# Kernel tuning notes

Measured on AMD Instinct MI355X. Metric: run time of the kernel, lower is better.

Reference implementation:

```python
import jax, jax.numpy as jnp
import numpy as np

jax.config.update("jax_enable_x64", True)  # module does int64 wraparound hashing

# Derived from BloomFilter(num_items=10_000_000, false_positive_rate=0.01):
#   pre-round num_bits = ceil(1e7 * ln(100) / ln(2)^2) ~= 95,850,584
#   num_hashes = ceil(pre_round_bits / 1e7 * ln(2)) = 7
#   num_bits rounded up to power of two -> 2**27
NUM_BITS = 2 ** 27
BIT_MASK = NUM_BITS - 1
NUM_HASHES = 7
PRIME = 2654435761


def _hash(values):
    """(N,) int64 -> (N, k) bit positions. Matches torch: (v*PRIME + seed) & bit_mask
    (note Python precedence: & binds looser than +). int64 overflow wraps identically."""
    seeds = jnp.arange(NUM_HASHES, dtype=jnp.int64)
    return (values[:, None] * PRIME + seeds[None, :]) & BIT_MASK


def setup_inputs() -> dict:
    key = jax.random.key(0)
    k1, k2 = jax.random.split(key)
    add_values = jax.random.randint(k1, (4_000_000,), 0, 2**31 - 1, dtype=jnp.int64)
    query_values = jax.random.randint(k2, (8_000_000,), 0, 2**31 - 1, dtype=jnp.int64)
    return {"add_values": add_values, "query_values": query_values}


def reference(add_values, query_values):
    # Bit array of NUM_BITS bools. Semantically identical to the packed int64
    # bitset: word w, offset b in torch <-> flat index (w << 6) | b here, and a
    # bitwise-OR of single-bit masks is exactly an idempotent set-True scatter.
    bits = jnp.zeros((NUM_BITS,), dtype=bool)

    # add(): scatter-set all k hash positions of every inserted value
    add_pos = _hash(add_values)  # (M, k)
    bits = bits.at[add_pos.reshape(-1)].set(True)

    # contains(): gather k bits per query and AND-reduce
    q_pos = _hash(query_values)  # (N, k)
    return jnp.all(bits[q_pos], axis=1)  # (N,) bool
```

## Files before the change

kernel.cpp:

```cpp
#include <hip/hip_runtime.h>
#include <stdint.h>


#define NUM_BITS_LOG2 27
#define NUM_BITS (1u << NUM_BITS_LOG2)
#define BIT_MASK (NUM_BITS - 1u)
#define NUM_WORDS (NUM_BITS >> 6)
#define WORD_MASK (NUM_WORDS - 1u)
#define PRIME 2654435761u
#define H_WORDS (NUM_WORDS >> 2)

#define NBUCKETS 512
#define BKT_SHIFT (NUM_BITS_LOG2 - 9)
#define REGION_WORDS (1u << (BKT_SHIFT - 6))
#define H_WORDS_PER_REGION (REGION_WORDS / 4)
#define CAP 8688u
#define CHUNK 8192u

typedef int vint4 __attribute__((ext_vector_type(4)));
typedef unsigned long long vull2 __attribute__((ext_vector_type(2)));

#define WS_H_ONLY 20971520ull
#define WS_FULL   38766592ull

__global__ __launch_bounds__(512) void scatter_kernel(
    const int* __restrict__ vals, int n,
    uint32_t* __restrict__ lists, uint32_t* __restrict__ gcnt)
{
    __shared__ uint32_t hist[NBUCKETS];
    __shared__ uint32_t cur[NBUCKETS];
    __shared__ uint32_t gdelta[NBUCKETS];
    __shared__ uint32_t wsum[8];
    __shared__ uint32_t wexc[8];
    __shared__ uint32_t total_s;
    __shared__ uint32_t sortbuf[CHUNK];
    const uint32_t tid = threadIdx.x;
    const uint32_t lane = tid & 63u;
    const uint32_t wv = tid >> 6;
    const uint32_t un = (uint32_t)n;
    const uint32_t nchunks = (un + CHUNK - 1u) / CHUNK;

    for (uint32_t c = blockIdx.x; c < nchunks; c += gridDim.x) {
        const uint32_t base = c * CHUNK;
        const bool full = (base + CHUNK <= un);

        hist[tid] = 0u;
        __syncthreads();

        vint4 vv[4];
        if (full) {
            const vint4* src = (const vint4*)(vals + base);
            #pragma unroll
            for (int k = 0; k < 4; ++k) vv[k] = src[(uint32_t)k * 512u + tid];
            #pragma unroll
            for (int k = 0; k < 4; ++k) {
                #pragma unroll
                for (int j = 0; j < 4; ++j) {
                    uint32_t p = ((uint32_t)vv[k][j] * PRIME) & BIT_MASK;
                    uint32_t b1 = p >> BKT_SHIFT;
                    atomicAdd(&hist[b1], 1u);
                    uint32_t b2 = ((p + 6u) & BIT_MASK) >> BKT_SHIFT;
                    if (b2 != b1) {
                        uint32_t s2 = atomicAdd(&gcnt[b2], 1u);
                        if (s2 < CAP) lists[b2 * CAP + s2] = p;
                    }
                }
            }
        } else {
            #pragma unroll
            for (int k = 0; k < 16; ++k) {
                uint32_t idx = base + (uint32_t)k * 512u + tid;
                if (idx < un) {
                    uint32_t p = ((uint32_t)vals[idx] * PRIME) & BIT_MASK;
                    uint32_t b1 = p >> BKT_SHIFT;
                    atomicAdd(&hist[b1], 1u);
                    uint32_t b2 = ((p + 6u) & BIT_MASK) >> BKT_SHIFT;
                    if (b2 != b1) {
                        uint32_t s2 = atomicAdd(&gcnt[b2], 1u);
                        if (s2 < CAP) lists[b2 * CAP + s2] = p;
                    }
                }
            }
        }
        __syncthreads();

        const uint32_t c0 = hist[tid];
        uint32_t x = c0;
        #pragma unroll
        for (uint32_t d = 1; d < 64; d <<= 1) {
            uint32_t y = __shfl_up(x, d, 64);
            if (lane >= d) x += y;
        }
        if (lane == 63u) wsum[wv] = x;
        __syncthreads();
        if (wv == 0) {
            uint32_t t8 = (lane < 8u) ? wsum[lane] : 0u;
            #pragma unroll
            for (uint32_t d = 1; d < 8; d <<= 1) {
                uint32_t y = __shfl_up(t8, d, 64);
                if (lane >= d) t8 += y;
            }
            if (lane < 8u) wexc[lane] = t8 - wsum[lane];
        }
        __syncthreads();
        const uint32_t inc = x + wexc[wv];
        const uint32_t lb = inc - c0;
        if (tid == NBUCKETS - 1) total_s = inc;

        uint32_t go = c0 ? atomicAdd(&gcnt[tid], c0) : 0u;
        cur[tid] = lb;
        gdelta[tid] = tid * CAP + go - lb;
        __syncthreads();

        if (full) {
            #pragma unroll
            for (int k = 0; k < 4; ++k) {
                #pragma unroll
                for (int j = 0; j < 4; ++j) {
                    uint32_t p = ((uint32_t)vv[k][j] * PRIME) & BIT_MASK;
                    uint32_t b1 = p >> BKT_SHIFT;
                    uint32_t s = atomicAdd(&cur[b1], 1u);
                    sortbuf[s] = p;
                }
            }
        } else {
            #pragma unroll
            for (int k = 0; k < 16; ++k) {
                uint32_t idx = base + (uint32_t)k * 512u + tid;
                if (idx < un) {
                    uint32_t p = ((uint32_t)vals[idx] * PRIME) & BIT_MASK;
                    uint32_t b1 = p >> BKT_SHIFT;
                    uint32_t s = atomicAdd(&cur[b1], 1u);
                    sortbuf[s] = p;
                }
            }
        }
        __syncthreads();

        const uint32_t total = total_s;
        for (uint32_t i = tid; i < total; i += 512u) {
            uint32_t p = sortbuf[i];
            uint32_t b = p >> BKT_SHIFT;
            uint32_t dst = gdelta[b] + i;
            if (dst - b * CAP < CAP) lists[dst] = p;
        }
        __syncthreads();
    }
}

__device__ __forceinline__ void set_window(unsigned long long* bm, uint32_t p, uint32_t b) {
    int d = (int)((p - (b << BKT_SHIFT)) & BIT_MASK);
    if (d >= (1 << 26)) d -= (1 << 27);
    if (d < -6 || d >= (1 << BKT_SHIFT)) return;
    if (d < 0) {
        atomicOr(&bm[0], 0x7Full >> (uint32_t)(-d));
    } else {
        uint32_t w = (uint32_t)d >> 6, s = (uint32_t)d & 63u;
        atomicOr(&bm[w], 0x7Full << s);
        if (s > 57u) atomicOr(&bm[w + 1], 0x7Full >> (64u - s));
    }
}

__device__ __forceinline__ unsigned long long nib16(unsigned long long a) {
    unsigned long long t = a & (a >> 1);
    unsigned long long u = t & (t >> 2);
    u &= 0x1111111111111111ull;
    u |= u >> 3;  u &= 0x0303030303030303ull;
    u |= u >> 6;  u &= 0x000F000F000F000Full;
    u |= u >> 12; u &= 0x000000FF000000FFull;
    u |= u >> 24; return u & 0xFFFFull;
}

__global__ __launch_bounds__(512) void build_bitmap_kernel(
    const uint32_t* __restrict__ lists, const uint32_t* __restrict__ gcnt,
    unsigned long long* __restrict__ bits, unsigned long long* __restrict__ H)
{
    __shared__ unsigned long long bm[REGION_WORDS + 1];
    const uint32_t b = blockIdx.x, tid = threadIdx.x;
    for (uint32_t i = tid; i < REGION_WORDS + 1; i += 512) bm[i] = 0ull;
    __syncthreads();

    const uint32_t m = min(gcnt[b], CAP);
    const uint32_t base = b * CAP;
    for (uint32_t i = tid; i < m; i += 512) set_window(bm, lists[base + i], b);
    __syncthreads();

    const uint32_t out_base = b * REGION_WORDS;
    for (uint32_t i = tid; i < REGION_WORDS / 2; i += 512) {
        vull2 w; w[0] = bm[i * 2]; w[1] = bm[i * 2 + 1];
        *((vull2*)(bits + out_base) + i) = w;
    }
    const uint32_t h_base = b * H_WORDS_PER_REGION;
    for (uint32_t i = tid; i < H_WORDS_PER_REGION; i += 512) {
        unsigned long long hw = nib16(bm[i * 4])
                              | (nib16(bm[i * 4 + 1]) << 16)
                              | (nib16(bm[i * 4 + 2]) << 32)
                              | (nib16(bm[i * 4 + 3]) << 48);
        H[h_base + i] = hw;
    }
}

__device__ __forceinline__ int query_one_branchy(uint32_t v,
                                                 const unsigned long long* __restrict__ bits) {
    uint32_t p = (v * PRIME) & BIT_MASK;
    uint32_t w = p >> 6, s = p & 63u;
    unsigned long long lo = bits[w];
    unsigned long long win;
    if (s <= 57u) win = lo >> s;
    else win = (lo >> s) | (bits[(w + 1u) & WORD_MASK] << (64u - s));
    return ((win & 0x7Full) == 0x7Full) ? 1 : 0;
}

__global__ __launch_bounds__(256) void query_kernelH(
    const int* __restrict__ vals, int n,
    const unsigned long long* __restrict__ bits,
    const uint32_t* __restrict__ H32, int* __restrict__ out)
{
    int t = blockIdx.x * 256 + threadIdx.x;
    int base = t * 8;
    if (base + 7 < n) {
        vint4 v0 = __builtin_nontemporal_load((const vint4*)(vals + base));
        vint4 v1 = __builtin_nontemporal_load((const vint4*)(vals + base + 4));
        uint32_t p[8], pass[8];
        #pragma unroll
        for (int j = 0; j < 4; ++j) {
            p[j]     = ((uint32_t)v0[j] * PRIME) & BIT_MASK;
            p[j + 4] = ((uint32_t)v1[j] * PRIME) & BIT_MASK;
        }
        #pragma unroll
        for (int j = 0; j < 8; ++j) {
            uint32_t m = ((p[j] + 3u) & BIT_MASK) >> 2;
            pass[j] = (H32[m >> 5] >> (m & 31u)) & 1u;
        }
        unsigned long long lo[8], hi[8];
        uint32_t w[8], s[8];
        #pragma unroll
        for (int j = 0; j < 8; ++j) {
            w[j] = p[j] >> 6; s[j] = p[j] & 63u;
            lo[j] = 0ull; hi[j] = 0ull;
            if (pass[j]) lo[j] = bits[w[j]];
        }
        #pragma unroll
        for (int j = 0; j < 8; ++j) {
            if (pass[j] && s[j] > 57u)
                hi[j] = bits[(w[j] + 1u) & WORD_MASK];
        }
        vint4 r0, r1;
        #pragma unroll
        for (int j = 0; j < 8; ++j) {
            unsigned long long win = (lo[j] >> s[j]) | ((hi[j] << 1) << (63u - s[j]));
            int r = ((win & 0x7Full) == 0x7Full) ? 1 : 0;
            if (j < 4) r0[j] = r; else r1[j - 4] = r;
        }
        __builtin_nontemporal_store(r0, (vint4*)(out + base));
        __builtin_nontemporal_store(r1, (vint4*)(out + base + 4));
    } else {
        for (int j = base; j < n; ++j)
            out[j] = query_one_branchy((uint32_t)vals[j], bits);
    }
}

__global__ __launch_bounds__(256) void zero_bits_kernel(vull2* __restrict__ bits, int n2) {
    int i = blockIdx.x * 256 + threadIdx.x;
    if (i < n2) { vull2 z = {0ull, 0ull}; __builtin_nontemporal_store(z, &bits[i]); }
}

__device__ __forceinline__ void insert_one_atomic(uint32_t v,
                                                  unsigned long long* __restrict__ bits) {
    uint32_t p = (v * PRIME) & BIT_MASK;
    uint32_t w = p >> 6, s = p & 63u;
    atomicOr(bits + w, 0x7Full << s);
    if (s > 57u) atomicOr(bits + ((w + 1u) & WORD_MASK), 0x7Full >> (64u - s));
}

__global__ __launch_bounds__(256) void insert_atomic_kernel(const int* __restrict__ vals, int n,
                                                            unsigned long long* __restrict__ bits) {
    int t = blockIdx.x * 256 + threadIdx.x;
    int base = t * 4;
    if (base + 3 < n) {
        vint4 v = __builtin_nontemporal_load((const vint4*)vals + t);
        insert_one_atomic((uint32_t)v.x, bits);
        insert_one_atomic((uint32_t)v.y, bits);
        insert_one_atomic((uint32_t)v.z, bits);
        insert_one_atomic((uint32_t)v.w, bits);
    } else {
        for (int j = base; j < n; ++j) insert_one_atomic((uint32_t)vals[j], bits);
    }
}

__global__ __launch_bounds__(256) void build_h_kernel(
    const unsigned long long* __restrict__ bits, unsigned long long* __restrict__ H)
{
    uint32_t i = blockIdx.x * 256 + threadIdx.x;
    const vull2* b2 = (const vull2*)bits + (size_t)i * 2;
    vull2 a = b2[0];
    vull2 b = b2[1];
    unsigned long long hw = nib16(a[0])
                          | (nib16(a[1]) << 16)
                          | (nib16(b[0]) << 32)
                          | (nib16(b[1]) << 48);
    H[i] = hw;
}

__global__ __launch_bounds__(256) void query_kernel8(
    const int* __restrict__ vals, int n,
    const unsigned long long* __restrict__ bits, int* __restrict__ out)
{
    int t = blockIdx.x * 256 + threadIdx.x;
    int base = t * 8;
    if (base + 7 < n) {
        vint4 v0 = __builtin_nontemporal_load((const vint4*)(vals + base));
        vint4 v1 = __builtin_nontemporal_load((const vint4*)(vals + base + 4));
        vint4 r0, r1;
        #pragma unroll
        for (int j = 0; j < 8; ++j) {
            uint32_t v = (uint32_t)(j < 4 ? v0[j] : v1[j - 4]);
            int r = query_one_branchy(v, bits);
            if (j < 4) r0[j] = r; else r1[j - 4] = r;
        }
        __builtin_nontemporal_store(r0, (vint4*)(out + base));
        __builtin_nontemporal_store(r1, (vint4*)(out + base + 4));
    } else {
        for (int j = base; j < n; ++j)
            out[j] = query_one_branchy((uint32_t)vals[j], bits);
    }
}

extern "C" void kernel_launch(void* const* d_in, const int* in_sizes, int n_in,
                              void* d_out, int out_size, void* d_ws, size_t ws_size,
                              hipStream_t stream) {
    const int* add_values   = (const int*)d_in[0];
    const int* query_values = (const int*)d_in[1];
    const int n_add   = in_sizes[0];
    const int n_query = in_sizes[1];
    int* out = (int*)d_out;

    uint8_t* ws = (uint8_t*)d_ws;
    unsigned long long* bits = (unsigned long long*)ws;
    unsigned long long* H    = (unsigned long long*)(ws + 16777216);
    uint32_t* lists = (uint32_t*)(ws + 20971520);
    uint32_t* gcnt  = (uint32_t*)(ws + 38764544);

    const int threads8 = (n_query + 7) / 8;

    if (ws_size >= WS_FULL) {
        const uint32_t nchunks = ((uint32_t)n_add + CHUNK - 1u) / CHUNK;
        hipMemsetAsync(gcnt, 0, NBUCKETS * sizeof(uint32_t), stream);
        scatter_kernel<<<nchunks, 512, 0, stream>>>(add_values, n_add, lists, gcnt);
        build_bitmap_kernel<<<NBUCKETS, 512, 0, stream>>>(lists, gcnt, bits, H);
        query_kernelH<<<(threads8 + 255) / 256, 256, 0, stream>>>(
            query_values, n_query, bits, (const uint32_t*)H, out);
    } else if (ws_size >= WS_H_ONLY) {
        const int n2 = NUM_WORDS / 2;
        zero_bits_kernel<<<(n2 + 255) / 256, 256, 0, stream>>>((vull2*)bits, n2);
        const int threads4 = (n_add + 3) / 4;
        insert_atomic_kernel<<<(threads4 + 255) / 256, 256, 0, stream>>>(
            add_values, n_add, bits);
        build_h_kernel<<<H_WORDS / 256, 256, 0, stream>>>(bits, H);
        query_kernelH<<<(threads8 + 255) / 256, 256, 0, stream>>>(
            query_values, n_query, bits, (const uint32_t*)H, out);
    } else {
        const int n2 = NUM_WORDS / 2;
        zero_bits_kernel<<<(n2 + 255) / 256, 256, 0, stream>>>((vull2*)bits, n2);
        const int threads4 = (n_add + 3) / 4;
        insert_atomic_kernel<<<(threads4 + 255) / 256, 256, 0, stream>>>(
            add_values, n_add, bits);
        query_kernel8<<<(threads8 + 255) / 256, 256, 0, stream>>>(
            query_values, n_query, bits, out);
    }
}
```

Baseline: 179.5 us.

## Fuse scatter, bitmap build and query into one persistent kernel with grid barriers

Replaces the three separate launches (bucket scatter, per-region bitmap build, query) with a single 512-block persistent kernel. The phases are separated by a software grid barrier built on agent-scope atomics. The two LDS layouts share storage through a union, and the query phase becomes a grid-stride loop. The goal is to remove launch gaps and tail effects between kernels. In exchange it adds barrier spin cost, depends on all 512 blocks being co-resident, and may cut occupancy and latency hiding in the random-access query phase.

Result: slower. 378.1 us (+110.6%).

```diff
diff --git a/kernel.cpp b/kernel.cpp
--- a/kernel.cpp
+++ b/kernel.cpp
@@ -16,136 +16,32 @@
 #define H_WORDS_PER_REGION (REGION_WORDS / 4)
 #define CAP 8688u
 #define CHUNK 8192u
+#define GRID_A 512
 
 typedef int vint4 __attribute__((ext_vector_type(4)));
 typedef unsigned long long vull2 __attribute__((ext_vector_type(2)));
 
 #define WS_H_ONLY 20971520ull
-#define WS_FULL   38766592ull
-
-__global__ __launch_bounds__(512) void scatter_kernel(
-    const int* __restrict__ vals, int n,
-    uint32_t* __restrict__ lists, uint32_t* __restrict__ gcnt)
-{
-    __shared__ uint32_t hist[NBUCKETS];
-    __shared__ uint32_t cur[NBUCKETS];
-    __shared__ uint32_t gdelta[NBUCKETS];
-    __shared__ uint32_t wsum[8];
-    __shared__ uint32_t wexc[8];
-    __shared__ uint32_t total_s;
-    __shared__ uint32_t sortbuf[CHUNK];
-    const uint32_t tid = threadIdx.x;
-    const uint32_t lane = tid & 63u;
-    const uint32_t wv = tid >> 6;
-    const uint32_t un = (uint32_t)n;
-    const uint32_t nchunks = (un + CHUNK - 1u) / CHUNK;
-
-    for (uint32_t c = blockIdx.x; c < nchunks; c += gridDim.x) {
-        const uint32_t base = c * CHUNK;
-        const bool full = (base + CHUNK <= un);
-
-        hist[tid] = 0u;
-        __syncthreads();
-
-        vint4 vv[4];
-        if (full) {
-            const vint4* src = (const vint4*)(vals + base);
-            #pragma unroll
-            for (int k = 0; k < 4; ++k) vv[k] = src[(uint32_t)k * 512u + tid];
-            #pragma unroll
-            for (int k = 0; k < 4; ++k) {
-                #pragma unroll
-                for (int j = 0; j < 4; ++j) {
-                    uint32_t p = ((uint32_t)vv[k][j] * PRIME) & BIT_MASK;
-                    uint32_t b1 = p >> BKT_SHIFT;
-                    atomicAdd(&hist[b1], 1u);
-                    uint32_t b2 = ((p + 6u) & BIT_MASK) >> BKT_SHIFT;
-                    if (b2 != b1) {
-                        uint32_t s2 = atomicAdd(&gcnt[b2], 1u);
-                        if (s2 < CAP) lists[b2 * CAP + s2] = p;
-                    }
-                }
-            }
+#define WS_FULL   38766656ull
+
+__device__ __forceinline__ void grid_bar(uint32_t* __restrict__ bar) {
+    __syncthreads();
+    if (threadIdx.x == 0) {
+        __threadfence();
+        uint32_t g = __hip_atomic_load(&bar[1], __ATOMIC_RELAXED, __HIP_MEMORY_SCOPE_AGENT);
+        uint32_t a = __hip_atomic_fetch_add(&bar[0], 1u, __ATOMIC_ACQ_REL,
+                                            __HIP_MEMORY_SCOPE_AGENT);
+        if (a + 1u == (uint32_t)GRID_A) {
+            __hip_atomic_store(&bar[0], 0u, __ATOMIC_RELAXED, __HIP_MEMORY_SCOPE_AGENT);
+            __hip_atomic_fetch_add(&bar[1], 1u, __ATOMIC_RELEASE, __HIP_MEMORY_SCOPE_AGENT);
         } else {
-            #pragma unroll
-            for (int k = 0; k < 16; ++k) {
-                uint32_t idx = base + (uint32_t)k * 512u + tid;
-                if (idx < un) {
-                    uint32_t p = ((uint32_t)vals[idx] * PRIME) & BIT_MASK;
-                    uint32_t b1 = p >> BKT_SHIFT;
-                    atomicAdd(&hist[b1], 1u);
-                    uint32_t b2 = ((p + 6u) & BIT_MASK) >> BKT_SHIFT;
-                    if (b2 != b1) {
-                        uint32_t s2 = atomicAdd(&gcnt[b2], 1u);
-                        if (s2 < CAP) lists[b2 * CAP + s2] = p;
-                    }
-                }
-            }
-        }
-        __syncthreads();
-
-        const uint32_t c0 = hist[tid];
-        uint32_t x = c0;
-        #pragma unroll
-        for (uint32_t d = 1; d < 64; d <<= 1) {
-            uint32_t y = __shfl_up(x, d, 64);
-            if (lane >= d) x += y;
-        }
-        if (lane == 63u) wsum[wv] = x;
-        __syncthreads();
-        if (wv == 0) {
-            uint32_t t8 = (lane < 8u) ? wsum[lane] : 0u;
-            #pragma unroll
-            for (uint32_t d = 1; d < 8; d <<= 1) {
-                uint32_t y = __shfl_up(t8, d, 64);
-                if (lane >= d) t8 += y;
-            }
-            if (lane < 8u) wexc[lane] = t8 - wsum[lane];
-        }
-        __syncthreads();
-        const uint32_t inc = x + wexc[wv];
-        const uint32_t lb = inc - c0;
-        if (tid == NBUCKETS - 1) total_s = inc;
-
-        uint32_t go = c0 ? atomicAdd(&gcnt[tid], c0) : 0u;
-        cur[tid] = lb;
-        gdelta[tid] = tid * CAP + go - lb;
-        __syncthreads();
-
-        if (full) {
-            #pragma unroll
-            for (int k = 0; k < 4; ++k) {
-                #pragma unroll
-                for (int j = 0; j < 4; ++j) {
-                    uint32_t p = ((uint32_t)vv[k][j] * PRIME) & BIT_MASK;
-                    uint32_t b1 = p >> BKT_SHIFT;
-                    uint32_t s = atomicAdd(&cur[b1], 1u);
-                    sortbuf[s] = p;
-                }
-            }
-        } else {
-            #pragma unroll
-            for (int k = 0; k < 16; ++k) {
-                uint32_t idx = base + (uint32_t)k * 512u + tid;
-                if (idx < un) {
-                    uint32_t p = ((uint32_t)vals[idx] * PRIME) & BIT_MASK;
-                    uint32_t b1 = p >> BKT_SHIFT;
-                    uint32_t s = atomicAdd(&cur[b1], 1u);
-                    sortbuf[s] = p;
-                }
-            }
-        }
-        __syncthreads();
-
-        const uint32_t total = total_s;
-        for (uint32_t i = tid; i < total; i += 512u) {
-            uint32_t p = sortbuf[i];
-            uint32_t b = p >> BKT_SHIFT;
-            uint32_t dst = gdelta[b] + i;
-            if (dst - b * CAP < CAP) lists[dst] = p;
-        }
-        __syncthreads();
-    }
+            while (__hip_atomic_load(&bar[1], __ATOMIC_ACQUIRE,
+                                     __HIP_MEMORY_SCOPE_AGENT) == g)
+                __builtin_amdgcn_s_sleep(16);
+        }
+        __threadfence();
+    }
+    __syncthreads();
 }
 
 __device__ __forceinline__ void set_window(unsigned long long* bm, uint32_t p, uint32_t b) {
@@ -171,35 +67,6 @@
     u |= u >> 24; return u & 0xFFFFull;
 }
 
-__global__ __launch_bounds__(512) void build_bitmap_kernel(
-    const uint32_t* __restrict__ lists, const uint32_t* __restrict__ gcnt,
-    unsigned long long* __restrict__ bits, unsigned long long* __restrict__ H)
-{
-    __shared__ unsigned long long bm[REGION_WORDS + 1];
-    const uint32_t b = blockIdx.x, tid = threadIdx.x;
-    for (uint32_t i = tid; i < REGION_WORDS + 1; i += 512) bm[i] = 0ull;
-    __syncthreads();
-
-    const uint32_t m = min(gcnt[b], CAP);
-    const uint32_t base = b * CAP;
-    for (uint32_t i = tid; i < m; i += 512) set_window(bm, lists[base + i], b);
-    __syncthreads();
-
-    const uint32_t out_base = b * REGION_WORDS;
-    for (uint32_t i = tid; i < REGION_WORDS / 2; i += 512) {
-        vull2 w; w[0] = bm[i * 2]; w[1] = bm[i * 2 + 1];
-        *((vull2*)(bits + out_base) + i) = w;
-    }
-    const uint32_t h_base = b * H_WORDS_PER_REGION;
-    for (uint32_t i = tid; i < H_WORDS_PER_REGION; i += 512) {
-        unsigned long long hw = nib16(bm[i * 4])
-                              | (nib16(bm[i * 4 + 1]) << 16)
-                              | (nib16(bm[i * 4 + 2]) << 32)
-                              | (nib16(bm[i * 4 + 3]) << 48);
-        H[h_base + i] = hw;
-    }
-}
-
 __device__ __forceinline__ int query_one_branchy(uint32_t v,
                                                  const unsigned long long* __restrict__ bits) {
     uint32_t p = (v * PRIME) & BIT_MASK;
@@ -211,52 +78,219 @@
     return ((win & 0x7Full) == 0x7Full) ? 1 : 0;
 }
 
-__global__ __launch_bounds__(256) void query_kernelH(
-    const int* __restrict__ vals, int n,
-    const unsigned long long* __restrict__ bits,
-    const uint32_t* __restrict__ H32, int* __restrict__ out)
+__global__ __launch_bounds__(512) void bloom_fused_kernel(
+    const int* __restrict__ add_vals, int n_add,
+    const int* __restrict__ qvals, int n_query,
+    uint32_t* __restrict__ lists, uint32_t* __restrict__ gcnt,
+    unsigned long long* __restrict__ bits, unsigned long long* __restrict__ H,
+    int* __restrict__ out, uint32_t* __restrict__ bar)
 {
-    int t = blockIdx.x * 256 + threadIdx.x;
-    int base = t * 8;
-    if (base + 7 < n) {
-        vint4 v0 = __builtin_nontemporal_load((const vint4*)(vals + base));
-        vint4 v1 = __builtin_nontemporal_load((const vint4*)(vals + base + 4));
-        uint32_t p[8], pass[8];
-        #pragma unroll
-        for (int j = 0; j < 4; ++j) {
-            p[j]     = ((uint32_t)v0[j] * PRIME) & BIT_MASK;
-            p[j + 4] = ((uint32_t)v1[j] * PRIME) & BIT_MASK;
-        }
-        #pragma unroll
-        for (int j = 0; j < 8; ++j) {
-            uint32_t m = ((p[j] + 3u) & BIT_MASK) >> 2;
-            pass[j] = (H32[m >> 5] >> (m & 31u)) & 1u;
-        }
-        unsigned long long lo[8], hi[8];
-        uint32_t w[8], s[8];
-        #pragma unroll
-        for (int j = 0; j < 8; ++j) {
-            w[j] = p[j] >> 6; s[j] = p[j] & 63u;
-            lo[j] = 0ull; hi[j] = 0ull;
-            if (pass[j]) lo[j] = bits[w[j]];
-        }
-        #pragma unroll
-        for (int j = 0; j < 8; ++j) {
-            if (pass[j] && s[j] > 57u)
-                hi[j] = bits[(w[j] + 1u) & WORD_MASK];
-        }
-        vint4 r0, r1;
-        #pragma unroll
-        for (int j = 0; j < 8; ++j) {
-            unsigned long long win = (lo[j] >> s[j]) | ((hi[j] << 1) << (63u - s[j]));
-            int r = ((win & 0x7Full) == 0x7Full) ? 1 : 0;
-            if (j < 4) r0[j] = r; else r1[j - 4] = r;
-        }
-        __builtin_nontemporal_store(r0, (vint4*)(out + base));
-        __builtin_nontemporal_store(r1, (vint4*)(out + base + 4));
-    } else {
-        for (int j = base; j < n; ++j)
-            out[j] = query_one_branchy((uint32_t)vals[j], bits);
+    __shared__ union {
+        struct {
+            uint32_t hist[NBUCKETS];
+            uint32_t cur[NBUCKETS];
+            uint32_t gdelta[NBUCKETS];
+            uint32_t wsum[8];
+            uint32_t wexc[8];
+            uint32_t total;
+            uint32_t sortbuf[CHUNK];
+        } a;
+        struct {
+            unsigned long long bm[REGION_WORDS + 1];
+        } b;
+    } sh;
+
+    const uint32_t tid = threadIdx.x;
+    const uint32_t lane = tid & 63u;
+    const uint32_t wv = tid >> 6;
+
+    {
+        const uint32_t un = (uint32_t)n_add;
+        const uint32_t nchunks = (un + CHUNK - 1u) / CHUNK;
+        for (uint32_t c = blockIdx.x; c < nchunks; c += gridDim.x) {
+            const uint32_t base = c * CHUNK;
+            const bool full = (base + CHUNK <= un);
+
+            sh.a.hist[tid] = 0u;
+            __syncthreads();
+
+            vint4 vv[4];
+            if (full) {
+                const vint4* src = (const vint4*)(add_vals + base);
+                #pragma unroll
+                for (int k = 0; k < 4; ++k) vv[k] = src[(uint32_t)k * 512u + tid];
+                #pragma unroll
+                for (int k = 0; k < 4; ++k) {
+                    #pragma unroll
+                    for (int j = 0; j < 4; ++j) {
+                        uint32_t p = ((uint32_t)vv[k][j] * PRIME) & BIT_MASK;
+                        uint32_t b1 = p >> BKT_SHIFT;
+                        atomicAdd(&sh.a.hist[b1], 1u);
+                        uint32_t b2 = ((p + 6u) & BIT_MASK) >> BKT_SHIFT;
+                        if (b2 != b1) {
+                            uint32_t s2 = atomicAdd(&gcnt[b2], 1u);
+                            if (s2 < CAP) lists[b2 * CAP + s2] = p;
+                        }
+                    }
+                }
+            } else {
+                #pragma unroll
+                for (int k = 0; k < 16; ++k) {
+                    uint32_t idx = base + (uint32_t)k * 512u + tid;
+                    if (idx < un) {
+                        uint32_t p = ((uint32_t)add_vals[idx] * PRIME) & BIT_MASK;
+                        uint32_t b1 = p >> BKT_SHIFT;
+                        atomicAdd(&sh.a.hist[b1], 1u);
+                        uint32_t b2 = ((p + 6u) & BIT_MASK) >> BKT_SHIFT;
+                        if (b2 != b1) {
+                            uint32_t s2 = atomicAdd(&gcnt[b2], 1u);
+                            if (s2 < CAP) lists[b2 * CAP + s2] = p;
+                        }
+                    }
+                }
+            }
+            __syncthreads();
+
+            const uint32_t c0 = sh.a.hist[tid];
+            uint32_t x = c0;
+            #pragma unroll
+            for (uint32_t d = 1; d < 64; d <<= 1) {
+                uint32_t y = __shfl_up(x, d, 64);
+                if (lane >= d) x += y;
+            }
+            if (lane == 63u) sh.a.wsum[wv] = x;
+            __syncthreads();
+            if (wv == 0) {
+                uint32_t t8 = (lane < 8u) ? sh.a.wsum[lane] : 0u;
+                #pragma unroll
+                for (uint32_t d = 1; d < 8; d <<= 1) {
+                    uint32_t y = __shfl_up(t8, d, 64);
+                    if (lane >= d) t8 += y;
+                }
+                if (lane < 8u) sh.a.wexc[lane] = t8 - sh.a.wsum[lane];
+            }
+            __syncthreads();
+            const uint32_t inc = x + sh.a.wexc[wv];
+            const uint32_t lb = inc - c0;
+            if (tid == NBUCKETS - 1) sh.a.total = inc;
+
+            uint32_t go = c0 ? atomicAdd(&gcnt[tid], c0) : 0u;
+            sh.a.cur[tid] = lb;
+            sh.a.gdelta[tid] = tid * CAP + go - lb;
+            __syncthreads();
+
+            if (full) {
+                #pragma unroll
+                for (int k = 0; k < 4; ++k) {
+                    #pragma unroll
+                    for (int j = 0; j < 4; ++j) {
+                        uint32_t p = ((uint32_t)vv[k][j] * PRIME) & BIT_MASK;
+                        uint32_t b1 = p >> BKT_SHIFT;
+                        uint32_t s = atomicAdd(&sh.a.cur[b1], 1u);
+                        sh.a.sortbuf[s] = p;
+                    }
+                }
+            } else {
+                #pragma unroll
+                for (int k = 0; k < 16; ++k) {
+                    uint32_t idx = base + (uint32_t)k * 512u + tid;
+                    if (idx < un) {
+                        uint32_t p = ((uint32_t)add_vals[idx] * PRIME) & BIT_MASK;
+                        uint32_t b1 = p >> BKT_SHIFT;
+                        uint32_t s = atomicAdd(&sh.a.cur[b1], 1u);
+                        sh.a.sortbuf[s] = p;
+                    }
+                }
+            }
+            __syncthreads();
+
+            const uint32_t total = sh.a.total;
+            for (uint32_t i = tid; i < total; i += 512u) {
+                uint32_t p = sh.a.sortbuf[i];
+                uint32_t b = p >> BKT_SHIFT;
+                uint32_t dst = sh.a.gdelta[b] + i;
+                if (dst - b * CAP < CAP) lists[dst] = p;
+            }
+            __syncthreads();
+        }
+    }
+
+    grid_bar(bar);
+
+    {
+        const uint32_t b = blockIdx.x;
+        for (uint32_t i = tid; i < REGION_WORDS + 1; i += 512) sh.b.bm[i] = 0ull;
+        __syncthreads();
+
+        const uint32_t m = min(gcnt[b], CAP);
+        const uint32_t base = b * CAP;
+        for (uint32_t i = tid; i < m; i += 512) set_window(sh.b.bm, lists[base + i], b);
+        __syncthreads();
+
+        const uint32_t out_base = b * REGION_WORDS;
+        for (uint32_t i = tid; i < REGION_WORDS / 2; i += 512) {
+            vull2 w; w[0] = sh.b.bm[i * 2]; w[1] = sh.b.bm[i * 2 + 1];
+            *((vull2*)(bits + out_base) + i) = w;
+        }
+        const uint32_t h_base = b * H_WORDS_PER_REGION;
+        for (uint32_t i = tid; i < H_WORDS_PER_REGION; i += 512) {
+            unsigned long long hw = nib16(sh.b.bm[i * 4])
+                                  | (nib16(sh.b.bm[i * 4 + 1]) << 16)
+                                  | (nib16(sh.b.bm[i * 4 + 2]) << 32)
+                                  | (nib16(sh.b.bm[i * 4 + 3]) << 48);
+            H[h_base + i] = hw;
+        }
+    }
+
+    grid_bar(bar);
+
+    {
+        const uint32_t* H32 = (const uint32_t*)H;
+        const uint32_t nthreads = gridDim.x * 512u;
+        const uint32_t items = ((uint32_t)n_query + 7u) / 8u;
+        for (uint32_t it = blockIdx.x * 512u + tid; it < items; it += nthreads) {
+            int base = (int)(it * 8u);
+            if (base + 7 < n_query) {
+                vint4 v0 = __builtin_nontemporal_load((const vint4*)(qvals + base));
+                vint4 v1 = __builtin_nontemporal_load((const vint4*)(qvals + base + 4));
+                uint32_t p[8], pass[8];
+                #pragma unroll
+                for (int j = 0; j < 4; ++j) {
+                    p[j]     = ((uint32_t)v0[j] * PRIME) & BIT_MASK;
+                    p[j + 4] = ((uint32_t)v1[j] * PRIME) & BIT_MASK;
+                }
+                #pragma unroll
+                for (int j = 0; j < 8; ++j) {
+                    uint32_t m = ((p[j] + 3u) & BIT_MASK) >> 2;
+                    pass[j] = (H32[m >> 5] >> (m & 31u)) & 1u;
+                }
+                unsigned long long lo[8], hi[8];
+                uint32_t w[8], s[8];
+                #pragma unroll
+                for (int j = 0; j < 8; ++j) {
+                    w[j] = p[j] >> 6; s[j] = p[j] & 63u;
+                    lo[j] = 0ull; hi[j] = 0ull;
+                    if (pass[j]) lo[j] = bits[w[j]];
+                }
+                #pragma unroll
+                for (int j = 0; j < 8; ++j) {
+                    if (pass[j] && s[j] > 57u)
+                        hi[j] = bits[(w[j] + 1u) & WORD_MASK];
+                }
+                vint4 r0, r1;
+                #pragma unroll
+                for (int j = 0; j < 8; ++j) {
+                    unsigned long long win = (lo[j] >> s[j]) | ((hi[j] << 1) << (63u - s[j]));
+                    int r = ((win & 0x7Full) == 0x7Full) ? 1 : 0;
+                    if (j < 4) r0[j] = r; else r1[j - 4] = r;
+                }
+                __builtin_nontemporal_store(r0, (vint4*)(out + base));
+                __builtin_nontemporal_store(r1, (vint4*)(out + base + 4));
+            } else {
+                for (int j = base; j < n_query; ++j)
+                    out[j] = query_one_branchy((uint32_t)qvals[j], bits);
+            }
+        }
     }
 }
 
@@ -302,6 +336,55 @@
     H[i] = hw;
 }
 
+__global__ __launch_bounds__(256) void query_kernelH(
+    const int* __restrict__ vals, int n,
+    const unsigned long long* __restrict__ bits,
+    const uint32_t* __restrict__ H32, int* __restrict__ out)
+{
+    int t = blockIdx.x * 256 + threadIdx.x;
+    int base = t * 8;
+    if (base + 7 < n) {
+        vint4 v0 = __builtin_nontemporal_load((const vint4*)(vals + base));
+        vint4 v1 = __builtin_nontemporal_load((const vint4*)(vals + base + 4));
+        uint32_t p[8], pass[8];
+        #pragma unroll
+        for (int j = 0; j < 4; ++j) {
+            p[j]     = ((uint32_t)v0[j] * PRIME) & BIT_MASK;
+            p[j + 4] = ((uint32_t)v1[j] * PRIME) & BIT_MASK;
+        }
+        #pragma unroll
+        for (int j = 0; j < 8; ++j) {
+            uint32_t m = ((p[j] + 3u) & BIT_MASK) >> 2;
+            pass[j] = (H32[m >> 5] >> (m & 31u)) & 1u;
+        }
+        unsigned long long lo[8], hi[8];
+        uint32_t w[8], s[8];
+        #pragma unroll
+        for (int j = 0; j < 8; ++j) {
+            w[j] = p[j] >> 6; s[j] = p[j] & 63u;
+            lo[j] = 0ull; hi[j] = 0ull;
+            if (pass[j]) lo[j] = bits[w[j]];
+        }
+        #pragma unroll
+        for (int j = 0; j < 8; ++j) {
+            if (pass[j] && s[j] > 57u)
+                hi[j] = bits[(w[j] + 1u) & WORD_MASK];
+        }
+        vint4 r0, r1;
+        #pragma unroll
+        for (int j = 0; j < 8; ++j) {
+            unsigned long long win = (lo[j] >> s[j]) | ((hi[j] << 1) << (63u - s[j]));
+            int r = ((win & 0x7Full) == 0x7Full) ? 1 : 0;
+            if (j < 4) r0[j] = r; else r1[j - 4] = r;
+        }
+        __builtin_nontemporal_store(r0, (vint4*)(out + base));
+        __builtin_nontemporal_store(r1, (vint4*)(out + base + 4));
+    } else {
+        for (int j = base; j < n; ++j)
+            out[j] = query_one_branchy((uint32_t)vals[j], bits);
+    }
+}
+
 __global__ __launch_bounds__(256) void query_kernel8(
     const int* __restrict__ vals, int n,
     const unsigned long long* __restrict__ bits, int* __restrict__ out)
@@ -340,16 +423,15 @@
     unsigned long long* H    = (unsigned long long*)(ws + 16777216);
     uint32_t* lists = (uint32_t*)(ws + 20971520);
     uint32_t* gcnt  = (uint32_t*)(ws + 38764544);
+    uint32_t* bar   = (uint32_t*)(ws + 38766592);
 
     const int threads8 = (n_query + 7) / 8;
 
     if (ws_size >= WS_FULL) {
-        const uint32_t nchunks = ((uint32_t)n_add + CHUNK - 1u) / CHUNK;
-        hipMemsetAsync(gcnt, 0, NBUCKETS * sizeof(uint32_t), stream);
-        scatter_kernel<<<nchunks, 512, 0, stream>>>(add_values, n_add, lists, gcnt);
-        build_bitmap_kernel<<<NBUCKETS, 512, 0, stream>>>(lists, gcnt, bits, H);
-        query_kernelH<<<(threads8 + 255) / 256, 256, 0, stream>>>(
-            query_values, n_query, bits, (const uint32_t*)H, out);
+        hipMemsetAsync(gcnt, 0, 2048 + 64, stream);
+        bloom_fused_kernel<<<GRID_A, 512, 0, stream>>>(
+            add_values, n_add, query_values, n_query,
+            lists, gcnt, bits, H, out, bar);
     } else if (ws_size >= WS_H_ONLY) {
         const int n2 = NUM_WORDS / 2;
         zero_bits_kernel<<<(n2 + 255) / 256, 256, 0, stream>>>((vull2*)bits, n2);
```
